# Kernel tuning notes

Hardware: AMD Instinct MI355X
Metric: run time of the kernel (lower is better)

The kernel has to match this reference:

```python
import jax, jax.numpy as jnp
import numpy as np

VS = 32000; VT = 32000; E = 128; H = 256  # H = 2*embedding_dim per module code
B = 32; S = 128; T = 64


def setup_inputs() -> dict:
    key = jax.random.key(0)
    ks = jax.random.split(key, 12)
    sc = 0.05
    return {
        "src": jax.random.randint(ks[0], (B, S), 0, VS),
        "trg": jax.random.randint(ks[1], (B, T), 0, VT),
        "emb_src": jax.random.normal(ks[2], (VS, E), jnp.float32) * sc,
        "Wih_e": jax.random.normal(ks[3], (4 * H, E), jnp.float32) * sc,
        "Whh_e": jax.random.normal(ks[4], (4 * H, H), jnp.float32) * sc,
        "b_e": jax.random.normal(ks[5], (4 * H,), jnp.float32) * sc,
        "emb_trg": jax.random.normal(ks[6], (VT, E), jnp.float32) * sc,
        "Wih_d": jax.random.normal(ks[7], (4 * H, E), jnp.float32) * sc,
        "Whh_d": jax.random.normal(ks[8], (4 * H, H), jnp.float32) * sc,
        "b_d": jax.random.normal(ks[9], (4 * H,), jnp.float32) * sc,
        "Wfc": jax.random.normal(ks[10], (VT, H), jnp.float32) * sc,
        "bfc": jax.random.normal(ks[11], (VT,), jnp.float32) * sc,
    }


def _lstm(x_tbe, h0, c0, Wih, Whh, b):
    """PyTorch-gate-order LSTM (i,f,g,o). x_tbe: [T,B,E]. Returns ((hT,cT), hs [T,B,H])."""
    def step(carry, x):
        h, c = carry
        g = x @ Wih.T + h @ Whh.T + b  # [B,4H]
        i, f, gg, o = jnp.split(g, 4, axis=-1)
        c = jax.nn.sigmoid(f) * c + jax.nn.sigmoid(i) * jnp.tanh(gg)
        h = jax.nn.sigmoid(o) * jnp.tanh(c)
        return (h, c), h
    return jax.lax.scan(step, (h0, c0), x_tbe)


def reference(src, trg, emb_src, Wih_e, Whh_e, b_e, emb_trg, Wih_d, Whh_d, b_d, Wfc, bfc):
    Bsz = src.shape[0]
    h0 = jnp.zeros((Bsz, H), jnp.float32)
    c0 = jnp.zeros((Bsz, H), jnp.float32)
    # Encoder: embed + LSTM over src
    xe = emb_src[src].transpose(1, 0, 2)  # [S,B,E]
    (hn, cn), _ = _lstm(xe, h0, c0, Wih_e, Whh_e, b_e)
    # Decoder with teacher forcing: inputs are trg[:, :-1]
    xd = emb_trg[trg[:, :-1]].transpose(1, 0, 2)  # [T-1,B,E]
    (hn, cn), hs = _lstm(xd, hn, cn, Wih_d, Whh_d, b_d)
    preds = jnp.einsum('tbh,vh->btv', hs, Wfc) + bfc  # [B,T-1,V]
    zeros0 = jnp.zeros((Bsz, 1, preds.shape[-1]), jnp.float32)
    prediction = jnp.concatenate([zeros0, preds], axis=1)  # [B,T,V]; slot 0 stays zero as in torch
    return prediction, hn, cn
```

## Files before the change

### kernel.cpp

```cpp
#include <hip/hip_runtime.h>
#include <hip/hip_bf16.h>

#define Bsz 32
#define Ssz 128
#define Tsz 64
#define TD  63
#define NSTEP 191
#define Esz 128
#define Hsz 256
#define G4  1024
#define Vsz 32000
#define NB  16

typedef __attribute__((ext_vector_type(8))) short short8;
typedef __attribute__((ext_vector_type(4))) float f32x4;

__device__ __forceinline__ unsigned short f2bf(float f) {
    union { float f; unsigned u; } v; v.f = f;
    unsigned u = v.u;
    unsigned r = u + 0x7FFFu + ((u >> 16) & 1u);
    return (unsigned short)(r >> 16);
}

__device__ __forceinline__ float rcpf(float x) { return __builtin_amdgcn_rcpf(x); }
__device__ __forceinline__ float sigm(float x) { return rcpf(1.f + __expf(-x)); }
__device__ __forceinline__ float tanh_fast(float x) { return 1.f - 2.f * rcpf(1.f + __expf(2.f * x)); }

__global__ void k_cvt(const float* __restrict__ src, unsigned short* __restrict__ dst, long n) {
    long i = (long)blockIdx.x * blockDim.x + threadIdx.x;
    long base = i * 8;
    if (base >= n) return;
    float4 f0 = ((const float4*)(src + base))[0];
    float4 f1 = ((const float4*)(src + base))[1];
    union { unsigned short u[8]; uint4 v; } r;
    r.u[0] = f2bf(f0.x); r.u[1] = f2bf(f0.y); r.u[2] = f2bf(f0.z); r.u[3] = f2bf(f0.w);
    r.u[4] = f2bf(f1.x); r.u[5] = f2bf(f1.y); r.u[6] = f2bf(f1.z); r.u[7] = f2bf(f1.w);
    *(uint4*)(dst + base) = r.v;
}

__global__ void __launch_bounds__(256) k_input(
        const int* __restrict__ src, const int* __restrict__ trg,
        const float* __restrict__ emb_src, const float* __restrict__ emb_trg,
        const float* __restrict__ Wih_e, const float* __restrict__ Wih_d,
        const float* __restrict__ b_e, const float* __restrict__ b_d,
        float* __restrict__ xW, unsigned* __restrict__ bar,
        unsigned* __restrict__ hbuf_dw) {
    const int t = blockIdx.y;
    const int nb = blockIdx.x;
    const int tid = threadIdx.x;
    const bool enc = (t < Ssz);
    const float* emb  = enc ? emb_src : emb_trg;
    const float* Wih  = enc ? Wih_e : Wih_d;
    const float* bias = enc ? b_e : b_d;

    __shared__ unsigned short a_lds[32][Esz + 8];

    {
        int b = tid >> 3, seg = tid & 7;
        int tok = enc ? src[b * Ssz + t] : trg[b * Tsz + (t - Ssz)];
        const float* row = emb + (long)tok * Esz + seg * 16;
        #pragma unroll
        for (int i = 0; i < 16; ++i)
            a_lds[b][seg * 16 + i] = f2bf(row[i]);
    }
    if (t == 0) {
        __hip_atomic_store(&hbuf_dw[nb * 256 + tid], 0u, __ATOMIC_RELAXED,
                           __HIP_MEMORY_SCOPE_AGENT);
        if (nb == 0) {
            __hip_atomic_store(&bar[tid], 0u, __ATOMIC_RELAXED, __HIP_MEMORY_SCOPE_AGENT);
            __hip_atomic_store(&bar[256 + tid], 0u, __ATOMIC_RELAXED, __HIP_MEMORY_SCOPE_AGENT);
        }
    }
    __syncthreads();

    const int w = tid >> 6, l = tid & 63;
    const int n = l & 15, q = l >> 4;
    const int col = nb * 64 + w * 16 + n;

    short8 bw[4];
    #pragma unroll
    for (int kt = 0; kt < 4; ++kt) {
        const float* wr = Wih + (long)col * Esz + kt * 32 + q * 8;
        short8 f;
        #pragma unroll
        for (int i = 0; i < 8; ++i) f[i] = (short)f2bf(wr[i]);
        bw[kt] = f;
    }
    f32x4 acc0 = {0.f,0.f,0.f,0.f}, acc1 = {0.f,0.f,0.f,0.f};
    #pragma unroll
    for (int kt = 0; kt < 4; ++kt) {
        int k0 = kt * 32 + q * 8;
        short8 a0 = *(const short8*)&a_lds[n][k0];
        short8 a1 = *(const short8*)&a_lds[16 + n][k0];
        acc0 = __builtin_amdgcn_mfma_f32_16x16x32_bf16(a0, bw[kt], acc0, 0, 0, 0);
        acc1 = __builtin_amdgcn_mfma_f32_16x16x32_bf16(a1, bw[kt], acc1, 0, 0, 0);
    }
    float bv = bias[col];
    float* o = xW + (long)t * (Bsz * G4);
    #pragma unroll
    for (int r = 0; r < 4; ++r) {
        int m = q * 4 + r;
        o[m * G4 + col]        = acc0[r] + bv;
        o[(16 + m) * G4 + col] = acc1[r] + bv;
    }
}

__global__ void __launch_bounds__(256) k_recur(
        const float* __restrict__ Whh_e, const float* __restrict__ Whh_d,
        const float* __restrict__ xW, unsigned* __restrict__ hbuf_dw,
        unsigned* __restrict__ hs_dw, float* __restrict__ out_tail,
        unsigned* __restrict__ bar) {
    const int nb = blockIdx.x, tid = threadIdx.x;
    const int w = tid >> 6, l = tid & 63, n = l & 15, q = l >> 4;
    const int jbase = nb * 16;
    const int grow = w * Hsz + jbase + n;

    __shared__ unsigned short h_lds[32][Hsz + 8];
    __shared__ float glds[4][32][17];

    short8 be[8], bd[8];
    #pragma unroll
    for (int kt = 0; kt < 8; ++kt) {
        const float* we = Whh_e + (long)grow * Hsz + kt * 32 + q * 8;
        const float* wd = Whh_d + (long)grow * Hsz + kt * 32 + q * 8;
        short8 fe, fd;
        #pragma unroll
        for (int i = 0; i < 8; ++i) { fe[i] = (short)f2bf(we[i]); fd[i] = (short)f2bf(wd[i]); }
        be[kt] = fe; bd[kt] = fd;
    }

    const int pb = tid >> 3, jp = tid & 7, j0 = 2 * jp;
    float c0 = 0.f, c1 = 0.f;

    for (int s = 0; s < NSTEP; ++s) {
        const float* xrow = xW + (long)s * (Bsz * G4) + pb * G4 + jbase + j0;
        float2 xg0 = *(const float2*)(xrow + 0 * Hsz);
        float2 xg1 = *(const float2*)(xrow + 1 * Hsz);
        float2 xg2 = *(const float2*)(xrow + 2 * Hsz);
        float2 xg3 = *(const float2*)(xrow + 3 * Hsz);

        if (tid < NB) {
            while (__hip_atomic_load(&bar[tid * 32], __ATOMIC_RELAXED,
                                     __HIP_MEMORY_SCOPE_AGENT) < (unsigned)s) {}
        }
        __syncthreads();

        {
            const unsigned long long* hsrc =
                (const unsigned long long*)hbuf_dw + (s & 1) * 2048;
            #pragma unroll
            for (int i = 0; i < 8; ++i) {
                int d2 = i * 256 + tid;
                unsigned long long v = __hip_atomic_load(hsrc + d2, __ATOMIC_RELAXED,
                                                         __HIP_MEMORY_SCOPE_AGENT);
                int b = d2 >> 6, cq = d2 & 63;
                *(unsigned long long*)((char*)&h_lds[0][0] + b * 528 + cq * 8) = v;
            }
        }
        __syncthreads();

        f32x4 acc0 = {0.f,0.f,0.f,0.f}, acc1 = {0.f,0.f,0.f,0.f};
        if (s < Ssz) {
            #pragma unroll
            for (int kt = 0; kt < 8; ++kt) {
                int k0 = kt * 32 + q * 8;
                short8 a0 = *(const short8*)&h_lds[n][k0];
                short8 a1 = *(const short8*)&h_lds[16 + n][k0];
                acc0 = __builtin_amdgcn_mfma_f32_16x16x32_bf16(a0, be[kt], acc0, 0, 0, 0);
                acc1 = __builtin_amdgcn_mfma_f32_16x16x32_bf16(a1, be[kt], acc1, 0, 0, 0);
            }
        } else {
            #pragma unroll
            for (int kt = 0; kt < 8; ++kt) {
                int k0 = kt * 32 + q * 8;
                short8 a0 = *(const short8*)&h_lds[n][k0];
                short8 a1 = *(const short8*)&h_lds[16 + n][k0];
                acc0 = __builtin_amdgcn_mfma_f32_16x16x32_bf16(a0, bd[kt], acc0, 0, 0, 0);
                acc1 = __builtin_amdgcn_mfma_f32_16x16x32_bf16(a1, bd[kt], acc1, 0, 0, 0);
            }
        }
        #pragma unroll
        for (int r = 0; r < 4; ++r) {
            glds[w][q * 4 + r][n]      = acc0[r];
            glds[w][16 + q * 4 + r][n] = acc1[r];
        }
        __syncthreads();

        float gi0 = glds[0][pb][j0] + xg0.x, gi1 = glds[0][pb][j0 + 1] + xg0.y;
        float gf0 = glds[1][pb][j0] + xg1.x, gf1 = glds[1][pb][j0 + 1] + xg1.y;
        float gg0 = glds[2][pb][j0] + xg2.x, gg1 = glds[2][pb][j0 + 1] + xg2.y;
        float go0 = glds[3][pb][j0] + xg3.x, go1 = glds[3][pb][j0 + 1] + xg3.y;
        c0 = sigm(gf0) * c0 + sigm(gi0) * tanh_fast(gg0);
        c1 = sigm(gf1) * c1 + sigm(gi1) * tanh_fast(gg1);
        float h0 = sigm(go0) * tanh_fast(c0);
        float h1 = sigm(go1) * tanh_fast(c1);

        unsigned pk = (unsigned)f2bf(h0) | ((unsigned)f2bf(h1) << 16);
        unsigned* hdst = hbuf_dw + ((s + 1) & 1) * 4096
                         + pb * 128 + (jbase >> 1) + jp;
        __hip_atomic_store(hdst, pk, __ATOMIC_RELAXED, __HIP_MEMORY_SCOPE_AGENT);
        if (s >= Ssz)
            hs_dw[((long)(s - Ssz) * Bsz + pb) * 128 + (jbase >> 1) + jp] = pk;
        if (s == NSTEP - 1) {
            int jc = jbase + j0;
            *(float2*)&out_tail[pb * Hsz + jc]             = make_float2(h0, h1);
            *(float2*)&out_tail[Bsz * Hsz + pb * Hsz + jc] = make_float2(c0, c1);
        }

        __syncthreads();
        if (tid == 0)
            __hip_atomic_store(&bar[nb * 32], (unsigned)(s + 1), __ATOMIC_RELAXED,
                               __HIP_MEMORY_SCOPE_AGENT);
    }
}

__global__ void __launch_bounds__(256) k_proj(
        const unsigned short* __restrict__ hs, const unsigned short* __restrict__ WfcB,
        const float* __restrict__ bfc, float* __restrict__ out) {
    const int vb = blockIdx.x;
    const int td = blockIdx.y;
    const int tid = threadIdx.x, w = tid >> 6, l = tid & 63, n = l & 15, q = l >> 4;

    __shared__ unsigned short a_lds[32][Hsz + 8];
    __shared__ unsigned short b_lds[256][Hsz + 8];

    {
        int b = tid >> 3, seg = tid & 7;
        const uint4* g = (const uint4*)(hs + ((long)td * Bsz + b) * Hsz);
        #pragma unroll
        for (int i = 0; i < 4; ++i)
            *(uint4*)&a_lds[b][i * 64 + seg * 8] = g[i * 8 + seg];
    }
    {
        const uint4* g = (const uint4*)(WfcB + (long)vb * 256 * Hsz);
        #pragma unroll 4
        for (int i = 0; i < 32; ++i) {
            int u = i * 256 + tid;
            int row = u >> 5;
            int kk = (u & 31) * 8;
            *(uint4*)&b_lds[row][kk] = g[u];
        }
    }
    __syncthreads();

    short8 af[2][8];
    #pragma unroll
    for (int kt = 0; kt < 8; ++kt) {
        int k0 = kt * 32 + q * 8;
        af[0][kt] = *(const short8*)&a_lds[n][k0];
        af[1][kt] = *(const short8*)&a_lds[16 + n][k0];
    }
    f32x4 acc[2][4];
    #pragma unroll
    for (int nt = 0; nt < 4; ++nt) { acc[0][nt] = (f32x4){0.f,0.f,0.f,0.f}; acc[1][nt] = (f32x4){0.f,0.f,0.f,0.f}; }

    #pragma unroll
    for (int nt = 0; nt < 4; ++nt) {
        int cl = w * 64 + nt * 16 + n;
        #pragma unroll
        for (int kt = 0; kt < 8; ++kt) {
            short8 bf = *(const short8*)&b_lds[cl][kt * 32 + q * 8];
            acc[0][nt] = __builtin_amdgcn_mfma_f32_16x16x32_bf16(af[0][kt], bf, acc[0][nt], 0, 0, 0);
            acc[1][nt] = __builtin_amdgcn_mfma_f32_16x16x32_bf16(af[1][kt], bf, acc[1][nt], 0, 0, 0);
        }
    }
    #pragma unroll
    for (int nt = 0; nt < 4; ++nt) {
        int col = vb * 256 + w * 64 + nt * 16 + n;
        float bv = bfc[col];
        #pragma unroll
        for (int mt = 0; mt < 2; ++mt) {
            #pragma unroll
            for (int r = 0; r < 4; ++r) {
                int b = mt * 16 + q * 4 + r;
                out[(long)b * (Tsz * Vsz) + (long)(td + 1) * Vsz + col] = acc[mt][nt][r] + bv;
            }
        }
    }
}

__global__ void k_zero0(float* __restrict__ out) {
    int i = blockIdx.x * 256 + threadIdx.x;
    int b = i / 8000;
    int c = i % 8000;
    ((float4*)(out + (long)b * (Tsz * Vsz)))[c] = make_float4(0.f, 0.f, 0.f, 0.f);
}

extern "C" void kernel_launch(void* const* d_in, const int* in_sizes, int n_in,
                              void* d_out, int out_size, void* d_ws, size_t ws_size,
                              hipStream_t stream) {
    const int*   src     = (const int*)d_in[0];
    const int*   trg     = (const int*)d_in[1];
    const float* emb_src = (const float*)d_in[2];
    const float* Wih_e   = (const float*)d_in[3];
    const float* Whh_e   = (const float*)d_in[4];
    const float* b_e     = (const float*)d_in[5];
    const float* emb_trg = (const float*)d_in[6];
    const float* Wih_d   = (const float*)d_in[7];
    const float* Whh_d   = (const float*)d_in[8];
    const float* b_d     = (const float*)d_in[9];
    const float* Wfc     = (const float*)d_in[10];
    const float* bfc     = (const float*)d_in[11];
    float* out = (float*)d_out;

    char* ws = (char*)d_ws;
    float*          xW   = (float*)ws;
    unsigned short* WfcB = (unsigned short*)(ws + 25034752);
    unsigned short* hs   = (unsigned short*)(ws + 41418752);
    unsigned*       hbuf = (unsigned*)(ws + 42450944);
    unsigned*       bar  = (unsigned*)(ws + 42483712);
    (void)ws_size;

    k_cvt<<<4000, 256, 0, stream>>>(Wfc, WfcB, 8192000L);
    k_input<<<dim3(16, 191), 256, 0, stream>>>(src, trg, emb_src, emb_trg,
                                               Wih_e, Wih_d, b_e, b_d, xW, bar, hbuf);
    k_recur<<<NB, 256, 0, stream>>>(Whh_e, Whh_d, xW, hbuf, (unsigned*)hs,
                                    out + 65536000L, bar);
    k_zero0<<<1000, 256, 0, stream>>>(out);
    k_proj<<<dim3(125, 63), 256, 0, stream>>>(hs, WfcB, bfc, out);
}
```

Measured before the change: 1.164 ms.

## Make LSTM recurrence wave-independent with per-wave barriers and direct register h loads

Each of the four waves in a block now owns four hidden units across all four gates, so the gate combine can stay within the wave and no block-wide __syncthreads is needed. Every wave spins on its own set of 64 per-wave barrier flags and publishes its own flag, where before one thread per block polled 16 block flags. The hidden state is loaded from global memory straight into MFMA operand registers instead of being staged through LDS. This removes the per-step block barriers and the LDS round trip from the serial recurrence, at the cost of 64 flags polled per wave and more redundant global loads of h.

```diff
diff --git a/kernel.cpp b/kernel.cpp
--- a/kernel.cpp
+++ b/kernel.cpp
@@ -14,6 +14,8 @@
 
 typedef __attribute__((ext_vector_type(8))) short short8;
 typedef __attribute__((ext_vector_type(4))) float f32x4;
+
+union U64x2 { unsigned long long u[2]; short8 s; };
 
 __device__ __forceinline__ unsigned short f2bf(float f) {
     union { float f; unsigned u; } v; v.f = f;
@@ -105,112 +107,106 @@
     }
 }
 
-__global__ void __launch_bounds__(256) k_recur(
+__global__ void __launch_bounds__(256, 1) k_recur(
         const float* __restrict__ Whh_e, const float* __restrict__ Whh_d,
         const float* __restrict__ xW, unsigned* __restrict__ hbuf_dw,
         unsigned* __restrict__ hs_dw, float* __restrict__ out_tail,
         unsigned* __restrict__ bar) {
     const int nb = blockIdx.x, tid = threadIdx.x;
-    const int w = tid >> 6, l = tid & 63, n = l & 15, q = l >> 4;
-    const int jbase = nb * 16;
-    const int grow = w * Hsz + jbase + n;
-
-    __shared__ unsigned short h_lds[32][Hsz + 8];
-    __shared__ float glds[4][32][17];
+    const int w = tid >> 6, l = tid & 63;
+    const int n = l & 15, q = l >> 4;
+    const int p = (l >> 2) & 3, g = l & 3;
+    const int JB = nb * 16 + w * 4;
+    const int fid = nb * 4 + w;
+
+    __shared__ float glds[4][16][35];
 
     short8 be[8], bd[8];
-    #pragma unroll
-    for (int kt = 0; kt < 8; ++kt) {
-        const float* we = Whh_e + (long)grow * Hsz + kt * 32 + q * 8;
-        const float* wd = Whh_d + (long)grow * Hsz + kt * 32 + q * 8;
-        short8 fe, fd;
-        #pragma unroll
-        for (int i = 0; i < 8; ++i) { fe[i] = (short)f2bf(we[i]); fd[i] = (short)f2bf(wd[i]); }
-        be[kt] = fe; bd[kt] = fd;
-    }
-
-    const int pb = tid >> 3, jp = tid & 7, j0 = 2 * jp;
-    float c0 = 0.f, c1 = 0.f;
+    {
+        const int R = g * Hsz + JB + p;
+        #pragma unroll
+        for (int kt = 0; kt < 8; ++kt) {
+            const float* we = Whh_e + (long)R * Hsz + kt * 32 + q * 8;
+            const float* wd = Whh_d + (long)R * Hsz + kt * 32 + q * 8;
+            short8 fe, fd;
+            #pragma unroll
+            for (int i = 0; i < 8; ++i) { fe[i] = (short)f2bf(we[i]); fd[i] = (short)f2bf(wd[i]); }
+            be[kt] = fe; bd[kt] = fd;
+        }
+    }
+
+    const int m = l >> 1, c0 = (l & 1) * 2, jc = JB + c0;
+    float cc0 = 0.f, cc1 = 0.f;
 
     for (int s = 0; s < NSTEP; ++s) {
-        const float* xrow = xW + (long)s * (Bsz * G4) + pb * G4 + jbase + j0;
+        const float* xrow = xW + (long)s * (Bsz * G4) + m * G4 + jc;
         float2 xg0 = *(const float2*)(xrow + 0 * Hsz);
         float2 xg1 = *(const float2*)(xrow + 1 * Hsz);
         float2 xg2 = *(const float2*)(xrow + 2 * Hsz);
         float2 xg3 = *(const float2*)(xrow + 3 * Hsz);
 
-        if (tid < NB) {
-            while (__hip_atomic_load(&bar[tid * 32], __ATOMIC_RELAXED,
-                                     __HIP_MEMORY_SCOPE_AGENT) < (unsigned)s) {}
-        }
-        __syncthreads();
-
-        {
-            const unsigned long long* hsrc =
-                (const unsigned long long*)hbuf_dw + (s & 1) * 2048;
-            #pragma unroll
-            for (int i = 0; i < 8; ++i) {
-                int d2 = i * 256 + tid;
-                unsigned long long v = __hip_atomic_load(hsrc + d2, __ATOMIC_RELAXED,
-                                                         __HIP_MEMORY_SCOPE_AGENT);
-                int b = d2 >> 6, cq = d2 & 63;
-                *(unsigned long long*)((char*)&h_lds[0][0] + b * 528 + cq * 8) = v;
-            }
-        }
-        __syncthreads();
+        while (__hip_atomic_load(&bar[l * 8], __ATOMIC_RELAXED,
+                                 __HIP_MEMORY_SCOPE_AGENT) < (unsigned)s) {}
+        asm volatile("" ::: "memory");
+
+        const unsigned long long* hp =
+            (const unsigned long long*)hbuf_dw + (s & 1) * 2048;
+        U64x2 ha[8], hb[8];
+        #pragma unroll
+        for (int kt = 0; kt < 8; ++kt) {
+            int o0 = (n << 6) + (kt << 3) + (q << 1);
+            int o1 = o0 + (16 << 6);
+            ha[kt].u[0] = __hip_atomic_load(hp + o0,     __ATOMIC_RELAXED, __HIP_MEMORY_SCOPE_AGENT);
+            ha[kt].u[1] = __hip_atomic_load(hp + o0 + 1, __ATOMIC_RELAXED, __HIP_MEMORY_SCOPE_AGENT);
+            hb[kt].u[0] = __hip_atomic_load(hp + o1,     __ATOMIC_RELAXED, __HIP_MEMORY_SCOPE_AGENT);
+            hb[kt].u[1] = __hip_atomic_load(hp + o1 + 1, __ATOMIC_RELAXED, __HIP_MEMORY_SCOPE_AGENT);
+        }
 
         f32x4 acc0 = {0.f,0.f,0.f,0.f}, acc1 = {0.f,0.f,0.f,0.f};
         if (s < Ssz) {
             #pragma unroll
             for (int kt = 0; kt < 8; ++kt) {
-                int k0 = kt * 32 + q * 8;
-                short8 a0 = *(const short8*)&h_lds[n][k0];
-                short8 a1 = *(const short8*)&h_lds[16 + n][k0];
-                acc0 = __builtin_amdgcn_mfma_f32_16x16x32_bf16(a0, be[kt], acc0, 0, 0, 0);
-                acc1 = __builtin_amdgcn_mfma_f32_16x16x32_bf16(a1, be[kt], acc1, 0, 0, 0);
+                acc0 = __builtin_amdgcn_mfma_f32_16x16x32_bf16(ha[kt].s, be[kt], acc0, 0, 0, 0);
+                acc1 = __builtin_amdgcn_mfma_f32_16x16x32_bf16(hb[kt].s, be[kt], acc1, 0, 0, 0);
             }
         } else {
             #pragma unroll
             for (int kt = 0; kt < 8; ++kt) {
-                int k0 = kt * 32 + q * 8;
-                short8 a0 = *(const short8*)&h_lds[n][k0];
-                short8 a1 = *(const short8*)&h_lds[16 + n][k0];
-                acc0 = __builtin_amdgcn_mfma_f32_16x16x32_bf16(a0, bd[kt], acc0, 0, 0, 0);
-                acc1 = __builtin_amdgcn_mfma_f32_16x16x32_bf16(a1, bd[kt], acc1, 0, 0, 0);
+                acc0 = __builtin_amdgcn_mfma_f32_16x16x32_bf16(ha[kt].s, bd[kt], acc0, 0, 0, 0);
+                acc1 = __builtin_amdgcn_mfma_f32_16x16x32_bf16(hb[kt].s, bd[kt], acc1, 0, 0, 0);
             }
         }
+
         #pragma unroll
         for (int r = 0; r < 4; ++r) {
-            glds[w][q * 4 + r][n]      = acc0[r];
-            glds[w][16 + q * 4 + r][n] = acc1[r];
-        }
-        __syncthreads();
-
-        float gi0 = glds[0][pb][j0] + xg0.x, gi1 = glds[0][pb][j0 + 1] + xg0.y;
-        float gf0 = glds[1][pb][j0] + xg1.x, gf1 = glds[1][pb][j0 + 1] + xg1.y;
-        float gg0 = glds[2][pb][j0] + xg2.x, gg1 = glds[2][pb][j0 + 1] + xg2.y;
-        float go0 = glds[3][pb][j0] + xg3.x, go1 = glds[3][pb][j0 + 1] + xg3.y;
-        c0 = sigm(gf0) * c0 + sigm(gi0) * tanh_fast(gg0);
-        c1 = sigm(gf1) * c1 + sigm(gi1) * tanh_fast(gg1);
-        float h0 = sigm(go0) * tanh_fast(c0);
-        float h1 = sigm(go1) * tanh_fast(c1);
+            glds[w][n][4 * q + r]      = acc0[r];
+            glds[w][n][16 + 4 * q + r] = acc1[r];
+        }
+        asm volatile("s_waitcnt lgkmcnt(0)" ::: "memory");
+
+        float ai0 = glds[w][4 * c0 + 0][m] + xg0.x, ai1 = glds[w][4 * c0 + 4][m] + xg0.y;
+        float af0 = glds[w][4 * c0 + 1][m] + xg1.x, af1 = glds[w][4 * c0 + 5][m] + xg1.y;
+        float ag0 = glds[w][4 * c0 + 2][m] + xg2.x, ag1 = glds[w][4 * c0 + 6][m] + xg2.y;
+        float ao0 = glds[w][4 * c0 + 3][m] + xg3.x, ao1 = glds[w][4 * c0 + 7][m] + xg3.y;
+        cc0 = sigm(af0) * cc0 + sigm(ai0) * tanh_fast(ag0);
+        cc1 = sigm(af1) * cc1 + sigm(ai1) * tanh_fast(ag1);
+        float h0 = sigm(ao0) * tanh_fast(cc0);
+        float h1 = sigm(ao1) * tanh_fast(cc1);
 
         unsigned pk = (unsigned)f2bf(h0) | ((unsigned)f2bf(h1) << 16);
-        unsigned* hdst = hbuf_dw + ((s + 1) & 1) * 4096
-                         + pb * 128 + (jbase >> 1) + jp;
-        __hip_atomic_store(hdst, pk, __ATOMIC_RELAXED, __HIP_MEMORY_SCOPE_AGENT);
+        __hip_atomic_store(hbuf_dw + ((s + 1) & 1) * 4096 + m * 128 + (jc >> 1),
+                           pk, __ATOMIC_RELAXED, __HIP_MEMORY_SCOPE_AGENT);
+        asm volatile("s_waitcnt vmcnt(0)" ::: "memory");
+        if (l == 0)
+            __hip_atomic_store(&bar[fid * 8], (unsigned)(s + 1), __ATOMIC_RELAXED,
+                               __HIP_MEMORY_SCOPE_AGENT);
+
         if (s >= Ssz)
-            hs_dw[((long)(s - Ssz) * Bsz + pb) * 128 + (jbase >> 1) + jp] = pk;
+            hs_dw[((long)(s - Ssz) * Bsz + m) * 128 + (jc >> 1)] = pk;
         if (s == NSTEP - 1) {
-            int jc = jbase + j0;
-            *(float2*)&out_tail[pb * Hsz + jc]             = make_float2(h0, h1);
-            *(float2*)&out_tail[Bsz * Hsz + pb * Hsz + jc] = make_float2(c0, c1);
-        }
-
-        __syncthreads();
-        if (tid == 0)
-            __hip_atomic_store(&bar[nb * 32], (unsigned)(s + 1), __ATOMIC_RELAXED,
-                               __HIP_MEMORY_SCOPE_AGENT);
+            *(float2*)&out_tail[m * Hsz + jc]             = make_float2(h0, h1);
+            *(float2*)&out_tail[Bsz * Hsz + m * Hsz + jc] = make_float2(cc0, cc1);
+        }
     }
 }
 
```

Result: slower. 1.753 ms (+50.6%).
